# Optimization experiments

Measured on AMD Instinct MI355X. Metric: run time of the kernel, lower is better.

## Reference

```python
import jax, jax.numpy as jnp
import numpy as np

E = 8          # num_experts
K = 2          # num_experts_per_tok
NORM_TOPK = True
B, S, D, F = 2, 1024, 2048, 1024  # batch, seq, hidden, moe_intermediate


def _kaiming_uniform(key, shape):
    # moe_fused_kaiming_uniform_: bound = sqrt(3*5 / in_features), in_features = shape[-1]
    bound = float(np.sqrt(3.0 * 5.0 / shape[-1]))
    return jax.random.uniform(key, shape, jnp.float32, -bound, bound)


def setup_inputs() -> dict:
    key = jax.random.key(0)
    k0, k1, k2, k3, k4 = jax.random.split(key, 5)
    gate_bound = float(1.0 / np.sqrt(D))  # nn.Linear default init
    return {
        "hidden_states": jax.random.normal(k0, (B, S, D), jnp.float32),
        "gate_w": jax.random.uniform(k1, (E, D), jnp.float32, -gate_bound, gate_bound),
        "w_gate_proj": _kaiming_uniform(k2, (E, F, D)),
        "w_up_proj": _kaiming_uniform(k3, (E, F, D)),
        "w_down_proj": _kaiming_uniform(k4, (E, D, F)),
    }


def reference(hidden_states, gate_w, w_gate_proj, w_up_proj, w_down_proj):
    b, s, d = hidden_states.shape
    x = hidden_states.reshape(-1, d)                      # [T, D]
    T = x.shape[0]

    # Router: softmax in fp32, top-k, optional renorm
    router_logits = x @ gate_w.T                          # [T, E]
    probs = jax.nn.softmax(router_logits.astype(jnp.float32), axis=-1)
    routing_weights, selected = jax.lax.top_k(probs, K)   # [T, K], [T, K]
    if NORM_TOPK:
        routing_weights = routing_weights / routing_weights.sum(-1, keepdims=True)
    routing_weights = routing_weights.astype(x.dtype)

    # Dense combine weights: c[t, e] = sum_k rw[t,k] * (sel[t,k]==e)
    combine = jnp.zeros((T, E), x.dtype).at[jnp.arange(T)[:, None], selected].add(routing_weights)

    # Expert SwiGLU FFN (dense over experts; combine zeros out unrouted experts,
    # identical math to sorted grouped-GEMM dispatch in the original)
    g = jnp.einsum('td,efd->tef', x, w_gate_proj)         # [T, E, F]
    u = jnp.einsum('td,efd->tef', x, w_up_proj)           # [T, E, F]
    h = jax.nn.silu(g) * u                                # [T, E, F]
    out = jnp.einsum('tef,edf,te->td', h, w_down_proj, combine)  # [T, D]

    return out.reshape(b, s, d), router_logits
```

## Files before the change

### kernel.cpp

```cpp
#include <hip/hip_runtime.h>
#include <stdint.h>

#define T_TOK 2048
#define DIM   2048
#define FDIM  1024
#define NE    8
#define MAXT128 40

typedef __attribute__((ext_vector_type(8))) short short8;
typedef __attribute__((ext_vector_type(4))) float f32x4;

__device__ __forceinline__ unsigned short f2b(float f) {
  union { float f; unsigned int i; } x; x.f = f;
  unsigned int r = x.i + 0x7fffu + ((x.i >> 16) & 1u);
  return (unsigned short)(r >> 16);
}

__device__ __forceinline__ void async16(void* lds, const void* g) {
  __builtin_amdgcn_global_load_lds(
      (const __attribute__((address_space(1))) void*)g,
      (__attribute__((address_space(3))) void*)lds, 16, 0, 0);
}

__device__ __forceinline__ void router_body(
    int t, const float* __restrict__ x, const float* __restrict__ gw,
    float* __restrict__ topkw, int* __restrict__ topke, int* __restrict__ counts,
    float* __restrict__ logits_out, unsigned short* __restrict__ xb)
{
  int lane = threadIdx.x & 63;
  const float* xr = x + (size_t)t * DIM;
  unsigned short* xbr = xb + (size_t)t * DIM;
  float acc[NE];
#pragma unroll
  for (int e = 0; e < NE; e++) acc[e] = 0.f;
  for (int d = lane * 4; d < DIM; d += 256) {
    float4 xv = *(const float4*)(xr + d);
    ushort4 xo;
    xo.x = f2b(xv.x); xo.y = f2b(xv.y); xo.z = f2b(xv.z); xo.w = f2b(xv.w);
    *(ushort4*)(xbr + d) = xo;
#pragma unroll
    for (int e = 0; e < NE; e++) {
      float4 gv = *(const float4*)(gw + e * DIM + d);
      acc[e] += xv.x * gv.x + xv.y * gv.y + xv.z * gv.z + xv.w * gv.w;
    }
  }
#pragma unroll
  for (int off = 32; off > 0; off >>= 1) {
#pragma unroll
    for (int e = 0; e < NE; e++) acc[e] += __shfl_down(acc[e], off);
  }
  if (lane == 0) {
    float m = acc[0];
#pragma unroll
    for (int e = 1; e < NE; e++) m = fmaxf(m, acc[e]);
    float p[NE];
#pragma unroll
    for (int e = 0; e < NE; e++) p[e] = __expf(acc[e] - m);
    int e0 = 0;
#pragma unroll
    for (int e = 1; e < NE; e++) if (acc[e] > acc[e0]) e0 = e;
    int e1 = -1;
#pragma unroll
    for (int e = 0; e < NE; e++) if (e != e0 && (e1 < 0 || acc[e] > acc[e1])) e1 = e;
    float s = p[e0] + p[e1];
    topkw[t * 2] = p[e0] / s;
    topkw[t * 2 + 1] = p[e1] / s;
    topke[t * 2] = e0; topke[t * 2 + 1] = e1;
    atomicAdd(&counts[e0], 1);
    atomicAdd(&counts[e1], 1);
#pragma unroll
    for (int e = 0; e < NE; e++) logits_out[t * NE + e] = acc[e];
  }
}

__device__ __forceinline__ void cvt_body(const float* __restrict__ src,
                                         unsigned short* __restrict__ dst, int bid)
{
  size_t i = ((size_t)bid * 256 + threadIdx.x) * 8;
  float4 a = *(const float4*)(src + i);
  float4 b = *(const float4*)(src + i + 4);
  ushort4 o0, o1;
  o0.x = f2b(a.x); o0.y = f2b(a.y); o0.z = f2b(a.z); o0.w = f2b(a.w);
  o1.x = f2b(b.x); o1.y = f2b(b.y); o1.z = f2b(b.z); o1.w = f2b(b.w);
  *(ushort4*)(dst + i) = o0;
  *(ushort4*)(dst + i + 4) = o1;
}

__global__ __launch_bounds__(256) void front_k(
    const float* __restrict__ x, const float* __restrict__ gw,
    float* __restrict__ topkw, int* __restrict__ topke, int* __restrict__ counts,
    float* __restrict__ logits_out, unsigned short* __restrict__ xb,
    const float* __restrict__ wg, unsigned short* __restrict__ wgb,
    const float* __restrict__ wu, unsigned short* __restrict__ wub,
    const float* __restrict__ wd, unsigned short* __restrict__ wdb)
{
  int bid = blockIdx.x;
  if (bid < 512) {
    int wave = threadIdx.x >> 6;
    router_body(bid * 4 + wave, x, gw, topkw, topke, counts, logits_out, xb);
  } else {
    bid -= 512;
    if (bid < 8192)       cvt_body(wg, wgb, bid);
    else if (bid < 16384) cvt_body(wu, wub, bid - 8192);
    else                  cvt_body(wd, wdb, bid - 16384);
  }
}

__global__ __launch_bounds__(256) void router_k(
    const float* __restrict__ x, const float* __restrict__ gw,
    float* __restrict__ topkw, int* __restrict__ topke, int* __restrict__ counts,
    float* __restrict__ logits_out, unsigned short* __restrict__ xb)
{
  int wave = threadIdx.x >> 6;
  router_body(blockIdx.x * 4 + wave, x, gw, topkw, topke, counts, logits_out, xb);
}

__global__ __launch_bounds__(256) void cvt2_k(const float* __restrict__ sA,
                                              unsigned short* __restrict__ dA,
                                              const float* __restrict__ sB,
                                              unsigned short* __restrict__ dB)
{
  int bid = blockIdx.x;
  if (bid < 8192) cvt_body(sA, dA, bid);
  else            cvt_body(sB, dB, bid - 8192);
}

__global__ __launch_bounds__(256) void cvt_w_k(const float* __restrict__ src,
                                               unsigned short* __restrict__ dst)
{
  cvt_body(src, dst, blockIdx.x);
}

__global__ __launch_bounds__(256) void scan_scatter_k(
    const int* __restrict__ counts, const int* __restrict__ topke,
    int4* __restrict__ tiles128, int* __restrict__ ntiles128,
    int* __restrict__ perm, int* __restrict__ slot_of)
{
  __shared__ int cur[NE];
  int tid = threadIdx.x;
  if (tid == 0) {
    int o = 0, nt2 = 0;
    for (int e = 0; e < NE; e++) {
      cur[e] = o;
      int c = counts[e];
      for (int r = 0; r < c; r += 128) {
        int rows = c - r < 128 ? c - r : 128;
        tiles128[nt2++] = make_int4(e, o + r, rows, 0);
      }
      o += c;
    }
    *ntiles128 = nt2;
  }
  __syncthreads();
  for (int i = tid; i < T_TOK * 2; i += 256) {
    int e = topke[i];
    int s = atomicAdd(&cur[e], 1);
    perm[s] = i;
    slot_of[i] = s;
  }
}


__global__ __launch_bounds__(256) void gemm1_bf_k(
    const unsigned short* __restrict__ xb,
    const unsigned short* __restrict__ wgb,
    const unsigned short* __restrict__ wub,
    const int* __restrict__ perm, const float* __restrict__ topkw,
    const int4* __restrict__ tiles, const int* __restrict__ ntiles,
    unsigned short* __restrict__ H)
{
  __shared__ short As[2][128 * 32];
  __shared__ short Bgs[2][64 * 32];
  __shared__ short Bus[2][64 * 32];
  __shared__ int rowtok[128];
  __shared__ float roww[128];

  if (blockIdx.y >= *ntiles) return;
  int4 tm = tiles[blockIdx.y];
  int e = tm.x, row0 = tm.y, nrows = tm.z;
  int tid = threadIdx.x;
  if (tid < 128) {
    int r = tid < nrows ? tid : (nrows - 1);
    int pid = perm[row0 + r];
    rowtok[tid] = pid >> 1;
    roww[tid] = topkw[pid];
  }
  __syncthreads();

  int f0 = blockIdx.x * 64;
  int crow = tid >> 2;
  int ccol = (tid & 3) * 8;
  const unsigned short* a0 = xb + (size_t)rowtok[crow] * DIM + ccol;
  const unsigned short* a1 = xb + (size_t)rowtok[crow + 64] * DIM + ccol;
  const unsigned short* bg = wgb + ((size_t)e * FDIM + f0 + crow) * DIM + ccol;
  const unsigned short* bu = wub + ((size_t)e * FDIM + f0 + crow) * DIM + ccol;

  int wave = tid >> 6, lane = tid & 63;
  int wm = wave >> 1, wn = wave & 1;
  int lrow = lane & 15, quad = lane >> 4;

  f32x4 accg[4][2], accu[4][2];
#pragma unroll
  for (int i = 0; i < 4; i++)
#pragma unroll
    for (int j = 0; j < 2; j++) {
      accg[i][j] = (f32x4){0.f, 0.f, 0.f, 0.f};
      accu[i][j] = (f32x4){0.f, 0.f, 0.f, 0.f};
    }

  const int aoff = (wm * 64 + lrow) * 32 + quad * 8;
  const int boff = (wn * 32 + lrow) * 32 + quad * 8;

#define STAGE1(b, k)                                 \
  do {                                               \
    async16(&As[b][tid * 8], a0 + (k));              \
    async16(&As[b][(256 + tid) * 8], a1 + (k));      \
    async16(&Bgs[b][tid * 8], bg + (k));             \
    async16(&Bus[b][tid * 8], bu + (k));             \
  } while (0)

  STAGE1(0, 0);

#pragma unroll 1
  for (int k0 = 0; k0 < DIM; k0 += 32) {
    int b = (k0 >> 5) & 1;
    __syncthreads();
    if (k0 + 32 < DIM) STAGE1(b ^ 1, k0 + 32);
    const short* arp = &As[0][0]  + b * (128 * 32) + aoff;
    const short* bgp = &Bgs[0][0] + b * (64 * 32) + boff;
    const short* bup = &Bus[0][0] + b * (64 * 32) + boff;
    short8 af[4], bgf[2], buf2[2];
#pragma unroll
    for (int i = 0; i < 4; i++) af[i] = *(const short8*)(arp + i * 16 * 32);
#pragma unroll
    for (int j = 0; j < 2; j++) {
      bgf[j]  = *(const short8*)(bgp + j * 16 * 32);
      buf2[j] = *(const short8*)(bup + j * 16 * 32);
    }
#pragma unroll
    for (int i = 0; i < 4; i++)
#pragma unroll
      for (int j = 0; j < 2; j++) {
        accg[i][j] = __builtin_amdgcn_mfma_f32_16x16x32_bf16(af[i], bgf[j], accg[i][j], 0, 0, 0);
        accu[i][j] = __builtin_amdgcn_mfma_f32_16x16x32_bf16(af[i], buf2[j], accu[i][j], 0, 0, 0);
      }
  }
#undef STAGE1

#pragma unroll
  for (int i = 0; i < 4; i++) {
#pragma unroll
    for (int reg = 0; reg < 4; reg++) {
      int r = wm * 64 + i * 16 + quad * 4 + reg;
      if (r < nrows) {
        float w = roww[r];
#pragma unroll
        for (int j = 0; j < 2; j++) {
          float g = accg[i][j][reg], u = accu[i][j][reg];
          float h = g * u * w / (1.f + __expf(-g));
          H[(size_t)(row0 + r) * FDIM + f0 + wn * 32 + j * 16 + lrow] = f2b(h);
        }
      }
    }
  }
}

__global__ __launch_bounds__(256) void gemm2_bf_k(
    const unsigned short* __restrict__ H,
    const unsigned short* __restrict__ wdb,
    const int4* __restrict__ tiles, const int* __restrict__ ntiles,
    float* __restrict__ O)
{
  __shared__ short Hs[2][128 * 32];
  __shared__ short Bs[2][128 * 32];

  if (blockIdx.y >= *ntiles) return;
  int4 tm = tiles[blockIdx.y];
  int e = tm.x, row0 = tm.y, nrows = tm.z;
  int tid = threadIdx.x;

  int d0 = blockIdx.x * 128;
  int crow = tid >> 2, ccol = (tid & 3) * 8;
  const unsigned short* a0 = H + (size_t)(row0 + crow) * FDIM + ccol;
  const unsigned short* a1 = H + (size_t)(row0 + crow + 64) * FDIM + ccol;
  const unsigned short* b0 = wdb + ((size_t)e * DIM + d0 + crow) * FDIM + ccol;
  const unsigned short* b1 = b0 + (size_t)64 * FDIM;

  int wave = tid >> 6, lane = tid & 63;
  int wm = wave >> 1, wn = wave & 1;
  int lrow = lane & 15, quad = lane >> 4;

  f32x4 acc[4][4];
#pragma unroll
  for (int i = 0; i < 4; i++)
#pragma unroll
    for (int j = 0; j < 4; j++) acc[i][j] = (f32x4){0.f, 0.f, 0.f, 0.f};

  const int aoff = (wm * 64 + lrow) * 32 + quad * 8;
  const int boff = (wn * 64 + lrow) * 32 + quad * 8;

#define STAGE2(b, k)                                 \
  do {                                               \
    async16(&Hs[b][tid * 8], a0 + (k));              \
    async16(&Hs[b][(256 + tid) * 8], a1 + (k));      \
    async16(&Bs[b][tid * 8], b0 + (k));              \
    async16(&Bs[b][(256 + tid) * 8], b1 + (k));      \
  } while (0)

  STAGE2(0, 0);

#pragma unroll 1
  for (int k0 = 0; k0 < FDIM; k0 += 32) {
    int b = (k0 >> 5) & 1;
    __syncthreads();
    if (k0 + 32 < FDIM) STAGE2(b ^ 1, k0 + 32);
    const short* arp = &Hs[0][0] + b * (128 * 32) + aoff;
    const short* brp = &Bs[0][0] + b * (128 * 32) + boff;
    short8 af[4], bf[4];
#pragma unroll
    for (int i = 0; i < 4; i++) af[i] = *(const short8*)(arp + i * 16 * 32);
#pragma unroll
    for (int j = 0; j < 4; j++) bf[j] = *(const short8*)(brp + j * 16 * 32);
#pragma unroll
    for (int i = 0; i < 4; i++)
#pragma unroll
      for (int j = 0; j < 4; j++)
        acc[i][j] = __builtin_amdgcn_mfma_f32_16x16x32_bf16(af[i], bf[j], acc[i][j], 0, 0, 0);
  }
#undef STAGE2

#pragma unroll
  for (int i = 0; i < 4; i++) {
#pragma unroll
    for (int reg = 0; reg < 4; reg++) {
      int r = wm * 64 + i * 16 + quad * 4 + reg;
      if (r < nrows) {
#pragma unroll
        for (int j = 0; j < 4; j++) {
          O[(size_t)(row0 + r) * DIM + d0 + wn * 64 + j * 16 + lrow] = acc[i][j][reg];
        }
      }
    }
  }
}

__global__ __launch_bounds__(256) void combine_k(
    const float* __restrict__ O, const int* __restrict__ slot_of,
    float* __restrict__ out)
{
  int t = blockIdx.x;
  int d = threadIdx.x * 8;
  int s0 = slot_of[2 * t], s1 = slot_of[2 * t + 1];
  const float4* p0 = (const float4*)(O + (size_t)s0 * DIM + d);
  const float4* p1 = (const float4*)(O + (size_t)s1 * DIM + d);
  float4 a0 = p0[0], a1 = p0[1], c0 = p1[0], c1 = p1[1];
  float4 r0, r1;
  r0.x = a0.x + c0.x; r0.y = a0.y + c0.y; r0.z = a0.z + c0.z; r0.w = a0.w + c0.w;
  r1.x = a1.x + c1.x; r1.y = a1.y + c1.y; r1.z = a1.z + c1.z; r1.w = a1.w + c1.w;
  float4* po = (float4*)(out + (size_t)t * DIM + d);
  po[0] = r0; po[1] = r1;
}


__global__ __launch_bounds__(256) void gemm1_f32_k(
    const unsigned short* __restrict__ xb,
    const float* __restrict__ wg,
    const float* __restrict__ wu,
    const int* __restrict__ perm, const float* __restrict__ topkw,
    const int4* __restrict__ tiles, const int* __restrict__ ntiles,
    unsigned short* __restrict__ H)
{
  __shared__ short As[128 * 32];
  __shared__ short Bgs[64 * 32];
  __shared__ short Bus[64 * 32];
  __shared__ int rowtok[128];
  __shared__ float roww[128];

  if (blockIdx.x >= *ntiles) return;
  int4 tm = tiles[blockIdx.x];
  int e = tm.x, row0 = tm.y, nrows = tm.z;
  int tid = threadIdx.x;
  if (tid < 128) {
    int r = tid < nrows ? tid : (nrows - 1);
    int pid = perm[row0 + r];
    rowtok[tid] = pid >> 1;
    roww[tid] = topkw[pid];
  }
  __syncthreads();

  int f0 = blockIdx.y * 64;
  int crow = tid >> 2;
  int ccol = (tid & 3) * 8;
  const unsigned short* a0 = xb + (size_t)rowtok[crow] * DIM + ccol;
  const unsigned short* a1 = xb + (size_t)rowtok[crow + 64] * DIM + ccol;
  const float* bg32 = wg + ((size_t)e * FDIM + f0 + crow) * DIM + ccol;
  const float* bu32 = wu + ((size_t)e * FDIM + f0 + crow) * DIM + ccol;
  short* as0 = As + tid * 8;
  short* as1 = As + (256 + tid) * 8;

  int wave = tid >> 6, lane = tid & 63;
  int wm = wave >> 1, wn = wave & 1;
  int lrow = lane & 15, quad = lane >> 4;

  f32x4 accg[4][2], accu[4][2];
#pragma unroll
  for (int i = 0; i < 4; i++)
#pragma unroll
    for (int j = 0; j < 2; j++) {
      accg[i][j] = (f32x4){0.f, 0.f, 0.f, 0.f};
      accu[i][j] = (f32x4){0.f, 0.f, 0.f, 0.f};
    }

  const short* arp = As + (wm * 64 + lrow) * 32 + quad * 8;
  const short* bgp = Bgs + (wn * 32 + lrow) * 32 + quad * 8;
  const short* bup = Bus + (wn * 32 + lrow) * 32 + quad * 8;

#pragma unroll 1
  for (int k0 = 0; k0 < DIM; k0 += 32) {
    async16(as0, a0 + k0);
    async16(as1, a1 + k0);
    float4 g0 = *(const float4*)(bg32 + k0);
    float4 g1 = *(const float4*)(bg32 + k0 + 4);
    float4 u0 = *(const float4*)(bu32 + k0);
    float4 u1 = *(const float4*)(bu32 + k0 + 4);
    short8 gs, us;
    gs[0] = f2b(g0.x); gs[1] = f2b(g0.y); gs[2] = f2b(g0.z); gs[3] = f2b(g0.w);
    gs[4] = f2b(g1.x); gs[5] = f2b(g1.y); gs[6] = f2b(g1.z); gs[7] = f2b(g1.w);
    us[0] = f2b(u0.x); us[1] = f2b(u0.y); us[2] = f2b(u0.z); us[3] = f2b(u0.w);
    us[4] = f2b(u1.x); us[5] = f2b(u1.y); us[6] = f2b(u1.z); us[7] = f2b(u1.w);
    *(short8*)(Bgs + tid * 8) = gs;
    *(short8*)(Bus + tid * 8) = us;
    __syncthreads();
    short8 af[4], bgf[2], buf2[2];
#pragma unroll
    for (int i = 0; i < 4; i++) af[i] = *(const short8*)(arp + i * 16 * 32);
#pragma unroll
    for (int j = 0; j < 2; j++) {
      bgf[j]  = *(const short8*)(bgp + j * 16 * 32);
      buf2[j] = *(const short8*)(bup + j * 16 * 32);
    }
#pragma unroll
    for (int i = 0; i < 4; i++)
#pragma unroll
      for (int j = 0; j < 2; j++) {
        accg[i][j] = __builtin_amdgcn_mfma_f32_16x16x32_bf16(af[i], bgf[j], accg[i][j], 0, 0, 0);
        accu[i][j] = __builtin_amdgcn_mfma_f32_16x16x32_bf16(af[i], buf2[j], accu[i][j], 0, 0, 0);
      }
    __syncthreads();
  }

#pragma unroll
  for (int i = 0; i < 4; i++) {
#pragma unroll
    for (int reg = 0; reg < 4; reg++) {
      int r = wm * 64 + i * 16 + quad * 4 + reg;
      if (r < nrows) {
        float w = roww[r];
#pragma unroll
        for (int j = 0; j < 2; j++) {
          float g = accg[i][j][reg], u = accu[i][j][reg];
          float h = g * u * w / (1.f + __expf(-g));
          H[(size_t)(row0 + r) * FDIM + f0 + wn * 32 + j * 16 + lrow] = f2b(h);
        }
      }
    }
  }
}

__global__ __launch_bounds__(256) void gemm2_f32_k(
    const unsigned short* __restrict__ H,
    const float* __restrict__ wd,
    const int* __restrict__ perm,
    const int4* __restrict__ tiles, const int* __restrict__ ntiles,
    float* __restrict__ out)
{
  __shared__ short Hs[128 * 32];
  __shared__ short Bs[64 * 32];
  __shared__ int rowtok[128];

  if (blockIdx.x >= *ntiles) return;
  int4 tm = tiles[blockIdx.x];
  int e = tm.x, row0 = tm.y, nrows = tm.z;
  int tid = threadIdx.x;
  if (tid < 128) {
    int r = tid < nrows ? tid : (nrows - 1);
    rowtok[tid] = perm[row0 + r] >> 1;
  }
  __syncthreads();

  int d0 = blockIdx.y * 64;
  int crow = tid >> 2, ccol = (tid & 3) * 8;
  const unsigned short* a0 = H + (size_t)(row0 + crow) * FDIM + ccol;
  const unsigned short* a1 = H + (size_t)(row0 + crow + 64) * FDIM + ccol;
  const float* b32 = wd + ((size_t)e * DIM + d0 + crow) * FDIM + ccol;
  short* hs0 = Hs + tid * 8;
  short* hs1 = Hs + (256 + tid) * 8;

  int wave = tid >> 6, lane = tid & 63;
  int wm = wave >> 1, wn = wave & 1;
  int lrow = lane & 15, quad = lane >> 4;

  f32x4 acc[4][2];
#pragma unroll
  for (int i = 0; i < 4; i++)
#pragma unroll
    for (int j = 0; j < 2; j++) acc[i][j] = (f32x4){0.f, 0.f, 0.f, 0.f};

  const short* arp = Hs + (wm * 64 + lrow) * 32 + quad * 8;
  const short* brp = Bs + (wn * 32 + lrow) * 32 + quad * 8;

#pragma unroll 1
  for (int k0 = 0; k0 < FDIM; k0 += 32) {
    async16(hs0, a0 + k0);
    async16(hs1, a1 + k0);
    float4 b0 = *(const float4*)(b32 + k0);
    float4 b1 = *(const float4*)(b32 + k0 + 4);
    short8 bsv;
    bsv[0] = f2b(b0.x); bsv[1] = f2b(b0.y); bsv[2] = f2b(b0.z); bsv[3] = f2b(b0.w);
    bsv[4] = f2b(b1.x); bsv[5] = f2b(b1.y); bsv[6] = f2b(b1.z); bsv[7] = f2b(b1.w);
    *(short8*)(Bs + tid * 8) = bsv;
    __syncthreads();
    short8 af[4], bf[2];
#pragma unroll
    for (int i = 0; i < 4; i++) af[i] = *(const short8*)(arp + i * 16 * 32);
#pragma unroll
    for (int j = 0; j < 2; j++) bf[j] = *(const short8*)(brp + j * 16 * 32);
#pragma unroll
    for (int i = 0; i < 4; i++)
#pragma unroll
      for (int j = 0; j < 2; j++)
        acc[i][j] = __builtin_amdgcn_mfma_f32_16x16x32_bf16(af[i], bf[j], acc[i][j], 0, 0, 0);
    __syncthreads();
  }

#pragma unroll
  for (int i = 0; i < 4; i++) {
#pragma unroll
    for (int reg = 0; reg < 4; reg++) {
      int r = wm * 64 + i * 16 + quad * 4 + reg;
      if (r < nrows) {
        int t = rowtok[r];
#pragma unroll
        for (int j = 0; j < 2; j++) {
          atomicAdd(&out[(size_t)t * DIM + d0 + wn * 32 + j * 16 + lrow], acc[i][j][reg]);
        }
      }
    }
  }
}

extern "C" void kernel_launch(void* const* d_in, const int* in_sizes, int n_in,
                              void* d_out, int out_size, void* d_ws, size_t ws_size,
                              hipStream_t stream)
{
  const float* x  = (const float*)d_in[0];
  const float* gw = (const float*)d_in[1];
  const float* wg = (const float*)d_in[2];
  const float* wu = (const float*)d_in[3];
  const float* wd = (const float*)d_in[4];
  float* out = (float*)d_out;
  float* logits_out = out + (size_t)T_TOK * DIM;

  char* ws = (char*)d_ws;
  float* topkw    = (float*)(ws + 0);
  int*   topke    = (int*)(ws + 16384);
  int*   counts   = (int*)(ws + 32768);
  int*   ntiles128= (int*)(ws + 32896);
  int4*  tiles128 = (int4*)(ws + 33024);
  int*   perm     = (int*)(ws + 35072);
  int*   slot_of  = (int*)(ws + 51456);
  unsigned short* xb  = (unsigned short*)(ws + 131072);
  unsigned short* H   = (unsigned short*)(ws + (9u  << 20));
  unsigned short* wgb = (unsigned short*)(ws + (18u << 20));
  unsigned short* wub = (unsigned short*)(ws + (50u << 20));
  const size_t WS_NEED_ALIAS = (size_t)82u  << 20;
  const size_t WS_NEED_FULL  = (size_t)146u << 20;

  hipMemsetAsync(counts, 0, 96, stream);

  if (ws_size >= WS_NEED_FULL) {
    unsigned short* wdb = (unsigned short*)(ws + (82u  << 20));
    float*          O   = (float*)         (ws + (114u << 20));
    front_k<<<512 + 24576, 256, 0, stream>>>(x, gw, topkw, topke, counts, logits_out, xb,
                                             wg, wgb, wu, wub, wd, wdb);
    scan_scatter_k<<<1, 256, 0, stream>>>(counts, topke, tiles128, ntiles128, perm, slot_of);
    gemm1_bf_k<<<dim3(FDIM / 64, MAXT128), 256, 0, stream>>>(xb, wgb, wub, perm, topkw, tiles128, ntiles128, H);
    gemm2_bf_k<<<dim3(DIM / 128, MAXT128), 256, 0, stream>>>(H, wdb, tiles128, ntiles128, O);
    combine_k<<<T_TOK, 256, 0, stream>>>(O, slot_of, out);
  } else if (ws_size >= WS_NEED_ALIAS) {
    unsigned short* wdb = wgb;
    float*          O   = (float*)(ws + (50u << 20));
    router_k<<<T_TOK / 4, 256, 0, stream>>>(x, gw, topkw, topke, counts, logits_out, xb);
    scan_scatter_k<<<1, 256, 0, stream>>>(counts, topke, tiles128, ntiles128, perm, slot_of);
    cvt2_k<<<16384, 256, 0, stream>>>(wg, wgb, wu, wub);
    gemm1_bf_k<<<dim3(FDIM / 64, MAXT128), 256, 0, stream>>>(xb, wgb, wub, perm, topkw, tiles128, ntiles128, H);
    cvt_w_k<<<8192, 256, 0, stream>>>(wd, wdb);
    gemm2_bf_k<<<dim3(DIM / 128, MAXT128), 256, 0, stream>>>(H, wdb, tiles128, ntiles128, O);
    combine_k<<<T_TOK, 256, 0, stream>>>(O, slot_of, out);
  } else {
    router_k<<<T_TOK / 4, 256, 0, stream>>>(x, gw, topkw, topke, counts, logits_out, xb);
    scan_scatter_k<<<1, 256, 0, stream>>>(counts, topke, tiles128, ntiles128, perm, slot_of);
    hipMemsetAsync(d_out, 0, (size_t)T_TOK * DIM * sizeof(float), stream);
    gemm1_f32_k<<<dim3(MAXT128, FDIM / 64), 256, 0, stream>>>(xb, wg, wu, perm, topkw, tiles128, ntiles128, H);
    gemm2_f32_k<<<dim3(MAXT128, DIM / 64), 256, 0, stream>>>(H, wd, perm, tiles128, ntiles128, out);
  }
}
```

Before: 368.5 us.

## Fuse gate/up weight bf16 conversion into GEMM1 and overlap down-proj conversion

The separate pre-pass that converted the gate and up weights to bf16 is removed. GEMM1 now loads fp32 weights directly, converts them in registers and writes bf16 tiles into LDS, prefetching one k-step ahead. Extra blocks appended to the GEMM1 grid convert the down-projection weights, so that work runs alongside the GEMM. This cuts a full fp32 read and bf16 write-back of two weight tensors, but doubles weight bytes per tile load and replaces async LDS loads with synchronous register staging. That adds VGPR pressure and the tile reads are repeated across token tiles.

```diff
diff --git a/kernel.cpp b/kernel.cpp
--- a/kernel.cpp
+++ b/kernel.cpp
@@ -22,12 +22,13 @@
       (__attribute__((address_space(3))) void*)lds, 16, 0, 0);
 }
 
-__device__ __forceinline__ void router_body(
-    int t, const float* __restrict__ x, const float* __restrict__ gw,
+__global__ __launch_bounds__(256) void router_k(
+    const float* __restrict__ x, const float* __restrict__ gw,
     float* __restrict__ topkw, int* __restrict__ topke, int* __restrict__ counts,
     float* __restrict__ logits_out, unsigned short* __restrict__ xb)
 {
-  int lane = threadIdx.x & 63;
+  int wave = threadIdx.x >> 6, lane = threadIdx.x & 63;
+  int t = blockIdx.x * 4 + wave;
   const float* xr = x + (size_t)t * DIM;
   unsigned short* xbr = xb + (size_t)t * DIM;
   float acc[NE];
@@ -71,64 +72,6 @@
 #pragma unroll
     for (int e = 0; e < NE; e++) logits_out[t * NE + e] = acc[e];
   }
-}
-
-__device__ __forceinline__ void cvt_body(const float* __restrict__ src,
-                                         unsigned short* __restrict__ dst, int bid)
-{
-  size_t i = ((size_t)bid * 256 + threadIdx.x) * 8;
-  float4 a = *(const float4*)(src + i);
-  float4 b = *(const float4*)(src + i + 4);
-  ushort4 o0, o1;
-  o0.x = f2b(a.x); o0.y = f2b(a.y); o0.z = f2b(a.z); o0.w = f2b(a.w);
-  o1.x = f2b(b.x); o1.y = f2b(b.y); o1.z = f2b(b.z); o1.w = f2b(b.w);
-  *(ushort4*)(dst + i) = o0;
-  *(ushort4*)(dst + i + 4) = o1;
-}
-
-__global__ __launch_bounds__(256) void front_k(
-    const float* __restrict__ x, const float* __restrict__ gw,
-    float* __restrict__ topkw, int* __restrict__ topke, int* __restrict__ counts,
-    float* __restrict__ logits_out, unsigned short* __restrict__ xb,
-    const float* __restrict__ wg, unsigned short* __restrict__ wgb,
-    const float* __restrict__ wu, unsigned short* __restrict__ wub,
-    const float* __restrict__ wd, unsigned short* __restrict__ wdb)
-{
-  int bid = blockIdx.x;
-  if (bid < 512) {
-    int wave = threadIdx.x >> 6;
-    router_body(bid * 4 + wave, x, gw, topkw, topke, counts, logits_out, xb);
-  } else {
-    bid -= 512;
-    if (bid < 8192)       cvt_body(wg, wgb, bid);
-    else if (bid < 16384) cvt_body(wu, wub, bid - 8192);
-    else                  cvt_body(wd, wdb, bid - 16384);
-  }
-}
-
-__global__ __launch_bounds__(256) void router_k(
-    const float* __restrict__ x, const float* __restrict__ gw,
-    float* __restrict__ topkw, int* __restrict__ topke, int* __restrict__ counts,
-    float* __restrict__ logits_out, unsigned short* __restrict__ xb)
-{
-  int wave = threadIdx.x >> 6;
-  router_body(blockIdx.x * 4 + wave, x, gw, topkw, topke, counts, logits_out, xb);
-}
-
-__global__ __launch_bounds__(256) void cvt2_k(const float* __restrict__ sA,
-                                              unsigned short* __restrict__ dA,
-                                              const float* __restrict__ sB,
-                                              unsigned short* __restrict__ dB)
-{
-  int bid = blockIdx.x;
-  if (bid < 8192) cvt_body(sA, dA, bid);
-  else            cvt_body(sB, dB, bid - 8192);
-}
-
-__global__ __launch_bounds__(256) void cvt_w_k(const float* __restrict__ src,
-                                               unsigned short* __restrict__ dst)
-{
-  cvt_body(src, dst, blockIdx.x);
 }
 
 __global__ __launch_bounds__(256) void scan_scatter_k(
@@ -160,11 +103,11 @@
   }
 }
 
-
-__global__ __launch_bounds__(256) void gemm1_bf_k(
+__global__ __launch_bounds__(256) void gemm1_k(
     const unsigned short* __restrict__ xb,
-    const unsigned short* __restrict__ wgb,
-    const unsigned short* __restrict__ wub,
+    const float* __restrict__ wg,
+    const float* __restrict__ wu,
+    const float* __restrict__ wd, unsigned short* __restrict__ wdb,
     const int* __restrict__ perm, const float* __restrict__ topkw,
     const int4* __restrict__ tiles, const int* __restrict__ ntiles,
     unsigned short* __restrict__ H)
@@ -175,10 +118,28 @@
   __shared__ int rowtok[128];
   __shared__ float roww[128];
 
+  int tid = threadIdx.x;
+
+  if (blockIdx.y >= MAXT128) {
+    int chunk = (blockIdx.y - MAXT128) * 16 + blockIdx.x;
+    size_t base = (size_t)chunk * 8192 + (size_t)tid * 8;
+#pragma unroll
+    for (int u = 0; u < 4; u++) {
+      size_t i = base + (size_t)u * 2048;
+      float4 a = *(const float4*)(wd + i);
+      float4 b = *(const float4*)(wd + i + 4);
+      ushort4 o0, o1;
+      o0.x = f2b(a.x); o0.y = f2b(a.y); o0.z = f2b(a.z); o0.w = f2b(a.w);
+      o1.x = f2b(b.x); o1.y = f2b(b.y); o1.z = f2b(b.z); o1.w = f2b(b.w);
+      *(ushort4*)(wdb + i) = o0;
+      *(ushort4*)(wdb + i + 4) = o1;
+    }
+    return;
+  }
+
   if (blockIdx.y >= *ntiles) return;
   int4 tm = tiles[blockIdx.y];
   int e = tm.x, row0 = tm.y, nrows = tm.z;
-  int tid = threadIdx.x;
   if (tid < 128) {
     int r = tid < nrows ? tid : (nrows - 1);
     int pid = perm[row0 + r];
@@ -192,8 +153,8 @@
   int ccol = (tid & 3) * 8;
   const unsigned short* a0 = xb + (size_t)rowtok[crow] * DIM + ccol;
   const unsigned short* a1 = xb + (size_t)rowtok[crow + 64] * DIM + ccol;
-  const unsigned short* bg = wgb + ((size_t)e * FDIM + f0 + crow) * DIM + ccol;
-  const unsigned short* bu = wub + ((size_t)e * FDIM + f0 + crow) * DIM + ccol;
+  const float* bg32 = wg + ((size_t)e * FDIM + f0 + crow) * DIM + ccol;
+  const float* bu32 = wu + ((size_t)e * FDIM + f0 + crow) * DIM + ccol;
 
   int wave = tid >> 6, lane = tid & 63;
   int wm = wave >> 1, wn = wave & 1;
@@ -211,24 +172,49 @@
   const int aoff = (wm * 64 + lrow) * 32 + quad * 8;
   const int boff = (wn * 32 + lrow) * 32 + quad * 8;
 
-#define STAGE1(b, k)                                 \
+#define PACK_WRITE(bb, G0, G1, U0, U1)               \
   do {                                               \
-    async16(&As[b][tid * 8], a0 + (k));              \
-    async16(&As[b][(256 + tid) * 8], a1 + (k));      \
-    async16(&Bgs[b][tid * 8], bg + (k));             \
-    async16(&Bus[b][tid * 8], bu + (k));             \
+    short8 gs, us;                                   \
+    gs[0]=f2b(G0.x); gs[1]=f2b(G0.y); gs[2]=f2b(G0.z); gs[3]=f2b(G0.w); \
+    gs[4]=f2b(G1.x); gs[5]=f2b(G1.y); gs[6]=f2b(G1.z); gs[7]=f2b(G1.w); \
+    us[0]=f2b(U0.x); us[1]=f2b(U0.y); us[2]=f2b(U0.z); us[3]=f2b(U0.w); \
+    us[4]=f2b(U1.x); us[5]=f2b(U1.y); us[6]=f2b(U1.z); us[7]=f2b(U1.w); \
+    *(short8*)(&Bgs[bb][tid * 8]) = gs;              \
+    *(short8*)(&Bus[bb][tid * 8]) = us;              \
   } while (0)
 
-  STAGE1(0, 0);
+  {
+    float4 g0 = *(const float4*)(bg32);
+    float4 g1 = *(const float4*)(bg32 + 4);
+    float4 u0 = *(const float4*)(bu32);
+    float4 u1 = *(const float4*)(bu32 + 4);
+    PACK_WRITE(0, g0, g1, u0, u1);
+  }
+  async16(&As[0][tid * 8], a0);
+  async16(&As[0][(256 + tid) * 8], a1);
+  float4 ng0 = *(const float4*)(bg32 + 32);
+  float4 ng1 = *(const float4*)(bg32 + 36);
+  float4 nu0 = *(const float4*)(bu32 + 32);
+  float4 nu1 = *(const float4*)(bu32 + 36);
 
 #pragma unroll 1
   for (int k0 = 0; k0 < DIM; k0 += 32) {
     int b = (k0 >> 5) & 1;
     __syncthreads();
-    if (k0 + 32 < DIM) STAGE1(b ^ 1, k0 + 32);
-    const short* arp = &As[0][0]  + b * (128 * 32) + aoff;
-    const short* bgp = &Bgs[0][0] + b * (64 * 32) + boff;
-    const short* bup = &Bus[0][0] + b * (64 * 32) + boff;
+    if (k0 + 32 < DIM) {
+      async16(&As[b ^ 1][tid * 8], a0 + k0 + 32);
+      async16(&As[b ^ 1][(256 + tid) * 8], a1 + k0 + 32);
+      PACK_WRITE(b ^ 1, ng0, ng1, nu0, nu1);
+    }
+    if (k0 + 64 < DIM) {
+      ng0 = *(const float4*)(bg32 + k0 + 64);
+      ng1 = *(const float4*)(bg32 + k0 + 68);
+      nu0 = *(const float4*)(bu32 + k0 + 64);
+      nu1 = *(const float4*)(bu32 + k0 + 68);
+    }
+    const short* arp = &As[b][0] + aoff;
+    const short* bgp = &Bgs[b][0] + boff;
+    const short* bup = &Bus[b][0] + boff;
     short8 af[4], bgf[2], buf2[2];
 #pragma unroll
     for (int i = 0; i < 4; i++) af[i] = *(const short8*)(arp + i * 16 * 32);
@@ -245,7 +231,7 @@
         accu[i][j] = __builtin_amdgcn_mfma_f32_16x16x32_bf16(af[i], buf2[j], accu[i][j], 0, 0, 0);
       }
   }
-#undef STAGE1
+#undef PACK_WRITE
 
 #pragma unroll
   for (int i = 0; i < 4; i++) {
@@ -571,35 +557,21 @@
   int*   slot_of  = (int*)(ws + 51456);
   unsigned short* xb  = (unsigned short*)(ws + 131072);
   unsigned short* H   = (unsigned short*)(ws + (9u  << 20));
-  unsigned short* wgb = (unsigned short*)(ws + (18u << 20));
-  unsigned short* wub = (unsigned short*)(ws + (50u << 20));
-  const size_t WS_NEED_ALIAS = (size_t)82u  << 20;
-  const size_t WS_NEED_FULL  = (size_t)146u << 20;
+  unsigned short* wdb = (unsigned short*)(ws + (18u << 20));
+  float*          O   = (float*)         (ws + (50u << 20));
+  const size_t WS_NEED = (size_t)82u << 20;
 
   hipMemsetAsync(counts, 0, 96, stream);
 
-  if (ws_size >= WS_NEED_FULL) {
-    unsigned short* wdb = (unsigned short*)(ws + (82u  << 20));
-    float*          O   = (float*)         (ws + (114u << 20));
-    front_k<<<512 + 24576, 256, 0, stream>>>(x, gw, topkw, topke, counts, logits_out, xb,
-                                             wg, wgb, wu, wub, wd, wdb);
-    scan_scatter_k<<<1, 256, 0, stream>>>(counts, topke, tiles128, ntiles128, perm, slot_of);
-    gemm1_bf_k<<<dim3(FDIM / 64, MAXT128), 256, 0, stream>>>(xb, wgb, wub, perm, topkw, tiles128, ntiles128, H);
-    gemm2_bf_k<<<dim3(DIM / 128, MAXT128), 256, 0, stream>>>(H, wdb, tiles128, ntiles128, O);
-    combine_k<<<T_TOK, 256, 0, stream>>>(O, slot_of, out);
-  } else if (ws_size >= WS_NEED_ALIAS) {
-    unsigned short* wdb = wgb;
-    float*          O   = (float*)(ws + (50u << 20));
-    router_k<<<T_TOK / 4, 256, 0, stream>>>(x, gw, topkw, topke, counts, logits_out, xb);
-    scan_scatter_k<<<1, 256, 0, stream>>>(counts, topke, tiles128, ntiles128, perm, slot_of);
-    cvt2_k<<<16384, 256, 0, stream>>>(wg, wgb, wu, wub);
-    gemm1_bf_k<<<dim3(FDIM / 64, MAXT128), 256, 0, stream>>>(xb, wgb, wub, perm, topkw, tiles128, ntiles128, H);
-    cvt_w_k<<<8192, 256, 0, stream>>>(wd, wdb);
+  router_k<<<T_TOK / 4, 256, 0, stream>>>(x, gw, topkw, topke, counts, logits_out, xb);
+  scan_scatter_k<<<1, 256, 0, stream>>>(counts, topke, tiles128, ntiles128, perm, slot_of);
+
+  if (ws_size >= WS_NEED) {
+    gemm1_k<<<dim3(FDIM / 64, MAXT128 + 128), 256, 0, stream>>>(
+        xb, wg, wu, wd, wdb, perm, topkw, tiles128, ntiles128, H);
     gemm2_bf_k<<<dim3(DIM / 128, MAXT128), 256, 0, stream>>>(H, wdb, tiles128, ntiles128, O);
     combine_k<<<T_TOK, 256, 0, stream>>>(O, slot_of, out);
   } else {
-    router_k<<<T_TOK / 4, 256, 0, stream>>>(x, gw, topkw, topke, counts, logits_out, xb);
-    scan_scatter_k<<<1, 256, 0, stream>>>(counts, topke, tiles128, ntiles128, perm, slot_of);
     hipMemsetAsync(d_out, 0, (size_t)T_TOK * DIM * sizeof(float), stream);
     gemm1_f32_k<<<dim3(MAXT128, FDIM / 64), 256, 0, stream>>>(xb, wg, wu, perm, topkw, tiles128, ntiles128, H);
     gemm2_f32_k<<<dim3(MAXT128, DIM / 64), 256, 0, stream>>>(H, wd, perm, tiles128, ntiles128, out);
```

Result: no change. 362.1 us (-1.8%).
